# Kernel optimization log

Hardware: AMD Instinct MI355X
Metric: run time of the kernel (lower is better)

## Reference

```python
import jax, jax.numpy as jnp
import numpy as np

EMBED_DIM = 768
NUM_HEADS = 12
HEAD_DIM = EMBED_DIM // NUM_HEADS


def setup_inputs() -> dict:
    key = jax.random.key(0)
    k_x, k_wqkv, k_bqkv, k_wo, k_bo = jax.random.split(key, 5)
    B, S, D = 4, 2048, EMBED_DIM
    bound = 1.0 / np.sqrt(D)
    x = jax.random.normal(k_x, (B, S, D), dtype=jnp.float32)
    # nn.Linear weights: torch stores [out, in]; we keep same layout and use x @ W.T
    W_qkv = jax.random.uniform(k_wqkv, (3 * D, D), jnp.float32, -bound, bound)
    b_qkv = jax.random.uniform(k_bqkv, (3 * D,), jnp.float32, -bound, bound)
    W_out = jax.random.uniform(k_wo, (D, D), jnp.float32, -bound, bound)
    b_out = jax.random.uniform(k_bo, (D,), jnp.float32, -bound, bound)
    return {"x": x, "W_qkv": W_qkv, "b_qkv": b_qkv, "W_out": W_out, "b_out": b_out}


def reference(x, W_qkv, b_qkv, W_out, b_out):
    B, S, D = x.shape
    H, Hd = NUM_HEADS, HEAD_DIM
    qkv = x @ W_qkv.T + b_qkv                       # [B,S,3D]
    qkv = qkv.reshape(B, S, H, 3 * Hd).transpose(0, 2, 1, 3)  # [B,H,S,3Hd]
    q, k, v = jnp.split(qkv, 3, axis=-1)            # each [B,H,S,Hd]
    scale = Hd ** -0.5
    scores = jnp.einsum("bhsd,bhtd->bhst", q, k) * scale  # [B,H,S,S]
    weights = jax.nn.softmax(scores, axis=-1)
    ctx = jnp.einsum("bhst,bhtd->bhsd", weights, v)       # [B,H,S,Hd]
    ctx = ctx.transpose(0, 2, 1, 3).reshape(B, S, D)      # [B,S,D]
    return ctx @ W_out.T + b_out
```

## Files before the change

### kernel.cpp

```cpp
#include <hip/hip_runtime.h>
#include <hip/hip_bf16.h>
#include <stdint.h>
#include <math.h>

typedef unsigned short u16;
typedef __attribute__((ext_vector_type(8))) short short8;
typedef __attribute__((ext_vector_type(4))) float f32x4;
typedef __attribute__((ext_vector_type(2))) unsigned int uint2v;

#define NB 4
#define NS 2048
#define NH 12
#define HD 64
#define ND 768
#define ND3 2304

#define QSCALE 0.18033688f

__device__ __forceinline__ u16 f2bf(float f) {
    unsigned int u = __float_as_uint(f);
    unsigned int r = u + 0x7fffu + ((u >> 16) & 1u);
    return (u16)(r >> 16);
}

typedef const __attribute__((address_space(1))) unsigned int gu32;
typedef __attribute__((address_space(3))) unsigned int lu32;
__device__ __forceinline__ void async16(const void* g, void* l) {
    __builtin_amdgcn_global_load_lds((gu32*)(uintptr_t)g, (lu32*)(uintptr_t)l, 16, 0, 0);
}

__global__ __launch_bounds__(256) void castk(const float* __restrict__ s, u16* __restrict__ d, int n4) {
    int i = blockIdx.x * 256 + threadIdx.x;
    if (i < n4) {
        float4 v = ((const float4*)s)[i];
        ushort4 o;
        o.x = f2bf(v.x); o.y = f2bf(v.y); o.z = f2bf(v.z); o.w = f2bf(v.w);
        ((ushort4*)d)[i] = o;
    }
}

__global__ __launch_bounds__(256) void gemm_qkv(const u16* __restrict__ A,
                                                const u16* __restrict__ Bw,
                                                const float* __restrict__ bias,
                                                u16* __restrict__ Qg,
                                                u16* __restrict__ Kg,
                                                u16* __restrict__ Vtg) {
    __shared__ u16 lds[8192];
    const int tid = threadIdx.x;
    const int w = tid >> 6, l = tid & 63;
    const int lam = l & 15, quad = l >> 4;
    const int wm = w >> 1, wn = w & 1;
    const int bm = blockIdx.x * 128, bn = blockIdx.y * 128;
    const int K = ND;

    f32x4 acc[4][4];
#pragma unroll
    for (int i = 0; i < 4; i++)
#pragma unroll
        for (int j = 0; j < 4; j++) { f32x4 z = {0.f, 0.f, 0.f, 0.f}; acc[i][j] = z; }

    const u16* gp[4];
    u16* sp[4];
#pragma unroll
    for (int i = 0; i < 4; i++) {
        int c = w * 4 + i;
        if (c < 8) { gp[i] = A + (size_t)(bm + c * 16 + lam) * K + quad * 8; sp[i] = lds + c * 512; }
        else { int nf = c - 8; gp[i] = Bw + (size_t)(bn + nf * 16 + lam) * K + quad * 8; sp[i] = lds + 4096 + nf * 512; }
    }

    for (int k0 = 0; k0 < K; k0 += 32) {
        __syncthreads();
#pragma unroll
        for (int i = 0; i < 4; i++) async16(gp[i] + k0, sp[i]);
        __syncthreads();
        short8 a[4], b[4];
#pragma unroll
        for (int i = 0; i < 4; i++) a[i] = *(const short8*)(lds + (wm * 4 + i) * 512 + l * 8);
#pragma unroll
        for (int i = 0; i < 4; i++) b[i] = *(const short8*)(lds + 4096 + (wn * 4 + i) * 512 + l * 8);
#pragma unroll
        for (int mf = 0; mf < 4; mf++)
#pragma unroll
            for (int nf = 0; nf < 4; nf++)
                acc[mf][nf] = __builtin_amdgcn_mfma_f32_16x16x32_bf16(a[mf], b[nf], acc[mf][nf], 0, 0, 0);
    }

#pragma unroll
    for (int nf = 0; nf < 4; nf++) {
        int n = bn + wn * 64 + nf * 16 + lam;
        float bv = bias[n];
        int hh = n / 192, rem = n % 192;
        int rgn = rem / 64, d = rem % 64;
        if (rgn == 2) {
#pragma unroll
            for (int mf = 0; mf < 4; mf++) {
                int m0 = bm + wm * 64 + mf * 16 + quad * 4;
                int bq = m0 >> 11, s0 = m0 & 2047;
                ushort4 o;
                o.x = f2bf(acc[mf][nf][0] + bv);
                o.y = f2bf(acc[mf][nf][1] + bv);
                o.z = f2bf(acc[mf][nf][2] + bv);
                o.w = f2bf(acc[mf][nf][3] + bv);
                *(ushort4*)(Vtg + ((size_t)((bq * NH + hh) * HD + d)) * NS + s0) = o;
            }
        } else {
            u16* dst = (rgn == 0) ? Qg : Kg;
            const float sc = (rgn == 0) ? QSCALE : 1.0f;
#pragma unroll
            for (int mf = 0; mf < 4; mf++)
#pragma unroll
                for (int r = 0; r < 4; r++) {
                    int m = bm + wm * 64 + mf * 16 + quad * 4 + r;
                    int bq = m >> 11, s = m & 2047;
                    dst[((size_t)((bq * NH + hh) * NS + s)) * HD + d] = f2bf((acc[mf][nf][r] + bv) * sc);
                }
        }
    }
}

__global__ __launch_bounds__(256, 3) void attn(const u16* __restrict__ Qg,
                                               const u16* __restrict__ Kg,
                                               const u16* __restrict__ Vtg,
                                               u16* __restrict__ ctx) {
    __shared__ u16 kt_lds[8192];
    __shared__ u16 vt_lds[8192];
    __shared__ u16 p_lds[9216];
    const int tid = threadIdx.x;
    const int w = tid >> 6, l = tid & 63;
    const int lam = l & 15, quad = l >> 4;
    const int qt = blockIdx.x, bh = blockIdx.y;
    const int b = bh / NH, hd = bh % NH;
    const u16* Qh = Qg + (size_t)bh * NS * HD;
    const u16* Kh = Kg + (size_t)bh * NS * HD;
    const u16* Vh = Vtg + (size_t)bh * HD * NS;

    const int qbase = qt * 128 + w * 32;
    short8 qf[2][2];
#pragma unroll
    for (int g = 0; g < 2; g++) {
        const u16* qp = Qh + (size_t)(qbase + g * 16 + lam) * HD + quad * 8;
        qf[g][0] = *(const short8*)(qp);
        qf[g][1] = *(const short8*)(qp + 32);
    }

    f32x4 ot[2][4];
#pragma unroll
    for (int g = 0; g < 2; g++)
#pragma unroll
        for (int i = 0; i < 4; i++) { f32x4 z = {0.f, 0.f, 0.f, 0.f}; ot[g][i] = z; }
    float lacc[2] = {0.f, 0.f};
    u16* pw = p_lds + w * 2304;

    const u16* kg[4];
    const u16* vg[4];
#pragma unroll
    for (int i = 0; i < 4; i++) {
        int cc = w * 4 + i, fgg = cc >> 1, ks = cc & 1;
        kg[i] = Kh + (size_t)(fgg * 16 + lam) * HD + ks * 32 + quad * 8;
        vg[i] = Vh + (size_t)(w * 16 + lam) * NS + i * 32 + quad * 8;
    }

    for (int kt = 0; kt < 16; kt++) {
        __syncthreads();
#pragma unroll
        for (int i = 0; i < 4; i++) { async16(kg[i], kt_lds + (w * 4 + i) * 512); kg[i] += 128 * HD; }
#pragma unroll
        for (int i = 0; i < 4; i++) { async16(vg[i], vt_lds + (w * 4 + i) * 512); vg[i] += 128; }
        __syncthreads();

#pragma unroll
        for (int hf = 0; hf < 2; hf++) {
            f32x4 st[2][4];
#pragma unroll
            for (int fg = 0; fg < 4; fg++) {
                const int cc = (hf * 4 + fg) * 2;
                short8 ka = *(const short8*)(kt_lds + (cc + 0) * 512 + l * 8);
                short8 kb = *(const short8*)(kt_lds + (cc + 1) * 512 + l * 8);
                f32x4 z0 = {0.f, 0.f, 0.f, 0.f};
                f32x4 z1 = {0.f, 0.f, 0.f, 0.f};
                z0 = __builtin_amdgcn_mfma_f32_16x16x32_bf16(ka, qf[0][0], z0, 0, 0, 0);
                z0 = __builtin_amdgcn_mfma_f32_16x16x32_bf16(kb, qf[0][1], z0, 0, 0, 0);
                z1 = __builtin_amdgcn_mfma_f32_16x16x32_bf16(ka, qf[1][0], z1, 0, 0, 0);
                z1 = __builtin_amdgcn_mfma_f32_16x16x32_bf16(kb, qf[1][1], z1, 0, 0, 0);
                st[0][fg] = z0;
                st[1][fg] = z1;
            }

#pragma unroll
            for (int g = 0; g < 2; g++) {
                u16* pr = pw + (g * 16 + lam) * 72;
                float ls = 0.f;
#pragma unroll
                for (int fg = 0; fg < 4; fg++) {
                    unsigned int u0 = __float_as_uint(__builtin_amdgcn_exp2f(st[g][fg][0]));
                    unsigned int u1 = __float_as_uint(__builtin_amdgcn_exp2f(st[g][fg][1]));
                    unsigned int u2 = __float_as_uint(__builtin_amdgcn_exp2f(st[g][fg][2]));
                    unsigned int u3 = __float_as_uint(__builtin_amdgcn_exp2f(st[g][fg][3]));
                    unsigned int t0 = u0 & 0xffff0000u, t1 = u1 & 0xffff0000u;
                    unsigned int t2 = u2 & 0xffff0000u, t3 = u3 & 0xffff0000u;
                    ls += (__uint_as_float(t0) + __uint_as_float(t1)) +
                          (__uint_as_float(t2) + __uint_as_float(t3));
                    uint2v pk;
                    pk.x = (u0 >> 16) | t1;
                    pk.y = (u2 >> 16) | t3;
                    *(uint2v*)(pr + fg * 16 + quad * 4) = pk;
                }
                lacc[g] += ls;
            }

            __builtin_amdgcn_s_waitcnt(0xc07f);

            short8 pf[2][2];
#pragma unroll
            for (int g = 0; g < 2; g++)
#pragma unroll
                for (int ks = 0; ks < 2; ks++)
                    pf[g][ks] = *(const short8*)(pw + (g * 16 + lam) * 72 + ks * 32 + quad * 8);

#pragma unroll
            for (int mf = 0; mf < 4; mf++)
#pragma unroll
                for (int ks = 0; ks < 2; ks++) {
                    short8 va = *(const short8*)(vt_lds + (mf * 4 + hf * 2 + ks) * 512 + l * 8);
                    ot[0][mf] = __builtin_amdgcn_mfma_f32_16x16x32_bf16(va, pf[0][ks], ot[0][mf], 0, 0, 0);
                    ot[1][mf] = __builtin_amdgcn_mfma_f32_16x16x32_bf16(va, pf[1][ks], ot[1][mf], 0, 0, 0);
                }
        }
    }

#pragma unroll
    for (int g = 0; g < 2; g++) {
        float lg = lacc[g];
        lg += __shfl_xor(lg, 16);
        lg += __shfl_xor(lg, 32);
        float inv = 1.0f / lg;
        const int t = qbase + g * 16 + lam;
        size_t obase = (size_t)(b * NS + t) * ND + hd * HD;
#pragma unroll
        for (int mf = 0; mf < 4; mf++) {
            ushort4 o;
            o.x = f2bf(ot[g][mf][0] * inv);
            o.y = f2bf(ot[g][mf][1] * inv);
            o.z = f2bf(ot[g][mf][2] * inv);
            o.w = f2bf(ot[g][mf][3] * inv);
            *(ushort4*)(ctx + obase + mf * 16 + quad * 4) = o;
        }
    }
}

__global__ __launch_bounds__(256) void gemm_out(const u16* __restrict__ A,
                                                const u16* __restrict__ Bw,
                                                const float* __restrict__ bias,
                                                float* __restrict__ out) {
    __shared__ u16 lds[8192];
    const int tid = threadIdx.x;
    const int w = tid >> 6, l = tid & 63;
    const int lam = l & 15, quad = l >> 4;
    const int wm = w >> 1, wn = w & 1;
    const int bm = blockIdx.x * 128, bn = blockIdx.y * 128;
    const int K = ND;

    f32x4 acc[4][4];
#pragma unroll
    for (int i = 0; i < 4; i++)
#pragma unroll
        for (int j = 0; j < 4; j++) { f32x4 z = {0.f, 0.f, 0.f, 0.f}; acc[i][j] = z; }

    const u16* gp[4];
    u16* sp[4];
#pragma unroll
    for (int i = 0; i < 4; i++) {
        int c = w * 4 + i;
        if (c < 8) { gp[i] = A + (size_t)(bm + c * 16 + lam) * K + quad * 8; sp[i] = lds + c * 512; }
        else { int nf = c - 8; gp[i] = Bw + (size_t)(bn + nf * 16 + lam) * K + quad * 8; sp[i] = lds + 4096 + nf * 512; }
    }

    for (int k0 = 0; k0 < K; k0 += 32) {
        __syncthreads();
#pragma unroll
        for (int i = 0; i < 4; i++) async16(gp[i] + k0, sp[i]);
        __syncthreads();
        short8 a[4], b[4];
#pragma unroll
        for (int i = 0; i < 4; i++) a[i] = *(const short8*)(lds + (wm * 4 + i) * 512 + l * 8);
#pragma unroll
        for (int i = 0; i < 4; i++) b[i] = *(const short8*)(lds + 4096 + (wn * 4 + i) * 512 + l * 8);
#pragma unroll
        for (int mf = 0; mf < 4; mf++)
#pragma unroll
            for (int nf = 0; nf < 4; nf++)
                acc[mf][nf] = __builtin_amdgcn_mfma_f32_16x16x32_bf16(a[mf], b[nf], acc[mf][nf], 0, 0, 0);
    }

#pragma unroll
    for (int nf = 0; nf < 4; nf++) {
        int n = bn + wn * 64 + nf * 16 + lam;
        float bv = bias[n];
#pragma unroll
        for (int mf = 0; mf < 4; mf++)
#pragma unroll
            for (int r = 0; r < 4; r++) {
                int m = bm + wm * 64 + mf * 16 + quad * 4 + r;
                out[(size_t)m * ND + n] = acc[mf][nf][r] + bv;
            }
    }
}

extern "C" void kernel_launch(void* const* d_in, const int* in_sizes, int n_in,
                              void* d_out, int out_size, void* d_ws, size_t ws_size,
                              hipStream_t stream) {
    const float* x    = (const float*)d_in[0];
    const float* Wqkv = (const float*)d_in[1];
    const float* bqkv = (const float*)d_in[2];
    const float* Wout = (const float*)d_in[3];
    const float* bout = (const float*)d_in[4];
    float* out = (float*)d_out;

    u16* p = (u16*)d_ws;
    u16* xb    = p; p += 6291456;
    u16* wqkvb = p; p += 1769472;
    u16* wob   = p; p += 589824;
    u16* Qg    = p; p += 6291456;
    u16* Kg    = p; p += 6291456;
    u16* Vtg   = p; p += 6291456;
    u16* ctx   = p; p += 6291456;

    castk<<<6144, 256, 0, stream>>>(x, xb, 1572864);
    castk<<<1728, 256, 0, stream>>>(Wqkv, wqkvb, 442368);
    castk<<<576, 256, 0, stream>>>(Wout, wob, 147456);
    gemm_qkv<<<dim3(64, 18), 256, 0, stream>>>(xb, wqkvb, bqkv, Qg, Kg, Vtg);
    attn<<<dim3(16, 48), 256, 0, stream>>>(Qg, Kg, Vtg, ctx);
    gemm_out<<<dim3(64, 6), 256, 0, stream>>>(ctx, wob, bout, out);
}
```

Measured before the change: 266.1 us.

## Rewrite attention with 32x32 MFMA tiles, register-resident P, and merged cast kernel

The attention kernel now uses 2 waves of 128 threads, each handling 64 query rows. Scores come from 32x32x16 MFMAs, and the exp'd probabilities feed the 32x32x8 PV MFMA straight from registers. This removes the LDS round trip for P and the waitcnt it required. The final row normalisation goes through a small LDS buffer, and the three cast launches are merged into one kernel. In exchange, register pressure per thread rises, each block has fewer waves to hide load latency, and the ctx stores become scalar 2-byte writes.

```diff
diff --git a/kernel.cpp b/kernel.cpp
--- a/kernel.cpp
+++ b/kernel.cpp
@@ -5,8 +5,9 @@
 
 typedef unsigned short u16;
 typedef __attribute__((ext_vector_type(8))) short short8;
+typedef __attribute__((ext_vector_type(4))) short short4v;
 typedef __attribute__((ext_vector_type(4))) float f32x4;
-typedef __attribute__((ext_vector_type(2))) unsigned int uint2v;
+typedef __attribute__((ext_vector_type(16))) float f32x16;
 
 #define NB 4
 #define NS 2048
@@ -29,14 +30,25 @@
     __builtin_amdgcn_global_load_lds((gu32*)(uintptr_t)g, (lu32*)(uintptr_t)l, 16, 0, 0);
 }
 
-__global__ __launch_bounds__(256) void castk(const float* __restrict__ s, u16* __restrict__ d, int n4) {
+#define XN4   1572864
+#define WQN4  442368
+#define WON4  147456
+__global__ __launch_bounds__(256) void castall(const float* __restrict__ x,
+                                               const float* __restrict__ wq,
+                                               const float* __restrict__ wo,
+                                               u16* __restrict__ xb,
+                                               u16* __restrict__ wqb,
+                                               u16* __restrict__ wob) {
     int i = blockIdx.x * 256 + threadIdx.x;
-    if (i < n4) {
-        float4 v = ((const float4*)s)[i];
-        ushort4 o;
-        o.x = f2bf(v.x); o.y = f2bf(v.y); o.z = f2bf(v.z); o.w = f2bf(v.w);
-        ((ushort4*)d)[i] = o;
-    }
+    const float* s; u16* d; int j;
+    if (i < XN4) { s = x; d = xb; j = i; }
+    else if (i < XN4 + WQN4) { s = wq; d = wqb; j = i - XN4; }
+    else if (i < XN4 + WQN4 + WON4) { s = wo; d = wob; j = i - XN4 - WQN4; }
+    else return;
+    float4 v = ((const float4*)s)[j];
+    ushort4 o;
+    o.x = f2bf(v.x); o.y = f2bf(v.y); o.z = f2bf(v.z); o.w = f2bf(v.w);
+    ((ushort4*)d)[j] = o;
 }
 
 __global__ __launch_bounds__(256) void gemm_qkv(const u16* __restrict__ A,
@@ -118,132 +130,116 @@
     }
 }
 
-__global__ __launch_bounds__(256, 3) void attn(const u16* __restrict__ Qg,
+__global__ __launch_bounds__(128, 2) void attn(const u16* __restrict__ Qg,
                                                const u16* __restrict__ Kg,
                                                const u16* __restrict__ Vtg,
                                                u16* __restrict__ ctx) {
     __shared__ u16 kt_lds[8192];
     __shared__ u16 vt_lds[8192];
-    __shared__ u16 p_lds[9216];
+    __shared__ float linv[128];
     const int tid = threadIdx.x;
-    const int w = tid >> 6, l = tid & 63;
-    const int lam = l & 15, quad = l >> 4;
+    const int w = tid >> 6, L = tid & 63;
+    const int r5 = L & 31, h = L >> 5;
     const int qt = blockIdx.x, bh = blockIdx.y;
     const int b = bh / NH, hd = bh % NH;
     const u16* Qh = Qg + (size_t)bh * NS * HD;
     const u16* Kh = Kg + (size_t)bh * NS * HD;
     const u16* Vh = Vtg + (size_t)bh * HD * NS;
 
-    const int qbase = qt * 128 + w * 32;
-    short8 qf[2][2];
-#pragma unroll
-    for (int g = 0; g < 2; g++) {
-        const u16* qp = Qh + (size_t)(qbase + g * 16 + lam) * HD + quad * 8;
-        qf[g][0] = *(const short8*)(qp);
-        qf[g][1] = *(const short8*)(qp + 32);
-    }
-
-    f32x4 ot[2][4];
-#pragma unroll
-    for (int g = 0; g < 2; g++)
-#pragma unroll
-        for (int i = 0; i < 4; i++) { f32x4 z = {0.f, 0.f, 0.f, 0.f}; ot[g][i] = z; }
+    const int qbase = qt * 128 + w * 64;
+
+    short8 qf[2][4];
+#pragma unroll
+    for (int ng = 0; ng < 2; ng++)
+#pragma unroll
+        for (int s = 0; s < 4; s++)
+            qf[ng][s] = *(const short8*)(Qh + (size_t)(qbase + ng * 32 + r5) * HD + s * 16 + h * 8);
+
+    f32x16 ot[2][2];
+#pragma unroll
+    for (int ng = 0; ng < 2; ng++)
+#pragma unroll
+        for (int hg = 0; hg < 2; hg++)
+#pragma unroll
+            for (int r = 0; r < 16; r++) ot[ng][hg][r] = 0.f;
     float lacc[2] = {0.f, 0.f};
-    u16* pw = p_lds + w * 2304;
-
-    const u16* kg[4];
-    const u16* vg[4];
-#pragma unroll
-    for (int i = 0; i < 4; i++) {
-        int cc = w * 4 + i, fgg = cc >> 1, ks = cc & 1;
-        kg[i] = Kh + (size_t)(fgg * 16 + lam) * HD + ks * 32 + quad * 8;
-        vg[i] = Vh + (size_t)(w * 16 + lam) * NS + i * 32 + quad * 8;
+
+    const u16* kgp[8];
+    const u16* vgp[8];
+#pragma unroll
+    for (int i = 0; i < 8; i++) {
+        int c = w * 8 + i, kg = c >> 2, s = c & 3;
+        kgp[i] = Kh + (size_t)(kg * 32 + r5) * HD + s * 16 + h * 8;
+        vgp[i] = Vh + (size_t)(w * 32 + r5) * NS + i * 16 + h * 8;
     }
 
     for (int kt = 0; kt < 16; kt++) {
         __syncthreads();
 #pragma unroll
-        for (int i = 0; i < 4; i++) { async16(kg[i], kt_lds + (w * 4 + i) * 512); kg[i] += 128 * HD; }
-#pragma unroll
-        for (int i = 0; i < 4; i++) { async16(vg[i], vt_lds + (w * 4 + i) * 512); vg[i] += 128; }
-        __syncthreads();
-
-#pragma unroll
-        for (int hf = 0; hf < 2; hf++) {
-            f32x4 st[2][4];
-#pragma unroll
-            for (int fg = 0; fg < 4; fg++) {
-                const int cc = (hf * 4 + fg) * 2;
-                short8 ka = *(const short8*)(kt_lds + (cc + 0) * 512 + l * 8);
-                short8 kb = *(const short8*)(kt_lds + (cc + 1) * 512 + l * 8);
-                f32x4 z0 = {0.f, 0.f, 0.f, 0.f};
-                f32x4 z1 = {0.f, 0.f, 0.f, 0.f};
-                z0 = __builtin_amdgcn_mfma_f32_16x16x32_bf16(ka, qf[0][0], z0, 0, 0, 0);
-                z0 = __builtin_amdgcn_mfma_f32_16x16x32_bf16(kb, qf[0][1], z0, 0, 0, 0);
-                z1 = __builtin_amdgcn_mfma_f32_16x16x32_bf16(ka, qf[1][0], z1, 0, 0, 0);
-                z1 = __builtin_amdgcn_mfma_f32_16x16x32_bf16(kb, qf[1][1], z1, 0, 0, 0);
-                st[0][fg] = z0;
-                st[1][fg] = z1;
-            }
-
-#pragma unroll
-            for (int g = 0; g < 2; g++) {
-                u16* pr = pw + (g * 16 + lam) * 72;
-                float ls = 0.f;
-#pragma unroll
-                for (int fg = 0; fg < 4; fg++) {
-                    unsigned int u0 = __float_as_uint(__builtin_amdgcn_exp2f(st[g][fg][0]));
-                    unsigned int u1 = __float_as_uint(__builtin_amdgcn_exp2f(st[g][fg][1]));
-                    unsigned int u2 = __float_as_uint(__builtin_amdgcn_exp2f(st[g][fg][2]));
-                    unsigned int u3 = __float_as_uint(__builtin_amdgcn_exp2f(st[g][fg][3]));
-                    unsigned int t0 = u0 & 0xffff0000u, t1 = u1 & 0xffff0000u;
-                    unsigned int t2 = u2 & 0xffff0000u, t3 = u3 & 0xffff0000u;
-                    ls += (__uint_as_float(t0) + __uint_as_float(t1)) +
-                          (__uint_as_float(t2) + __uint_as_float(t3));
-                    uint2v pk;
-                    pk.x = (u0 >> 16) | t1;
-                    pk.y = (u2 >> 16) | t3;
-                    *(uint2v*)(pr + fg * 16 + quad * 4) = pk;
+        for (int i = 0; i < 8; i++) { async16(kgp[i], kt_lds + (w * 8 + i) * 512); kgp[i] += 128 * HD; }
+#pragma unroll
+        for (int i = 0; i < 8; i++) { async16(vgp[i], vt_lds + (w * 8 + i) * 512); vgp[i] += 128; }
+        __syncthreads();
+
+#pragma unroll
+        for (int kg = 0; kg < 4; kg++) {
+            f32x16 st[2];
+#pragma unroll
+            for (int r = 0; r < 16; r++) { st[0][r] = 0.f; st[1][r] = 0.f; }
+#pragma unroll
+            for (int s = 0; s < 4; s++) {
+                short8 kf = *(const short8*)(kt_lds + (kg * 4 + s) * 512 + L * 8);
+                st[0] = __builtin_amdgcn_mfma_f32_32x32x16_bf16(kf, qf[0][s], st[0], 0, 0, 0);
+                st[1] = __builtin_amdgcn_mfma_f32_32x32x16_bf16(kf, qf[1][s], st[1], 0, 0, 0);
+            }
+
+#pragma unroll
+            for (int t4 = 0; t4 < 4; t4++) {
+                short4v pf[2];
+#pragma unroll
+                for (int ng = 0; ng < 2; ng++) {
+                    unsigned int u0 = __float_as_uint(__builtin_amdgcn_exp2f(st[ng][4 * t4 + 0]));
+                    unsigned int u1 = __float_as_uint(__builtin_amdgcn_exp2f(st[ng][4 * t4 + 1]));
+                    unsigned int u2 = __float_as_uint(__builtin_amdgcn_exp2f(st[ng][4 * t4 + 2]));
+                    unsigned int u3 = __float_as_uint(__builtin_amdgcn_exp2f(st[ng][4 * t4 + 3]));
+                    lacc[ng] += (__uint_as_float(u0 & 0xffff0000u) + __uint_as_float(u1 & 0xffff0000u)) +
+                                (__uint_as_float(u2 & 0xffff0000u) + __uint_as_float(u3 & 0xffff0000u));
+                    short4v p;
+                    p.x = (short)(u0 >> 16); p.y = (short)(u1 >> 16);
+                    p.z = (short)(u2 >> 16); p.w = (short)(u3 >> 16);
+                    pf[ng] = p;
                 }
-                lacc[g] += ls;
-            }
-
-            __builtin_amdgcn_s_waitcnt(0xc07f);
-
-            short8 pf[2][2];
-#pragma unroll
-            for (int g = 0; g < 2; g++)
-#pragma unroll
-                for (int ks = 0; ks < 2; ks++)
-                    pf[g][ks] = *(const short8*)(pw + (g * 16 + lam) * 72 + ks * 32 + quad * 8);
-
-#pragma unroll
-            for (int mf = 0; mf < 4; mf++)
-#pragma unroll
-                for (int ks = 0; ks < 2; ks++) {
-                    short8 va = *(const short8*)(vt_lds + (mf * 4 + hf * 2 + ks) * 512 + l * 8);
-                    ot[0][mf] = __builtin_amdgcn_mfma_f32_16x16x32_bf16(va, pf[0][ks], ot[0][mf], 0, 0, 0);
-                    ot[1][mf] = __builtin_amdgcn_mfma_f32_16x16x32_bf16(va, pf[1][ks], ot[1][mf], 0, 0, 0);
+                const int t = kg * 4 + t4;
+#pragma unroll
+                for (int hg = 0; hg < 2; hg++) {
+                    short4v vf = *(const short4v*)(vt_lds + hg * 4096 + t * 256 + r5 * 8 + h * 4);
+                    ot[0][hg] = __builtin_amdgcn_mfma_f32_32x32x8bf16_1k(pf[0], vf, ot[0][hg], 0, 0, 0);
+                    ot[1][hg] = __builtin_amdgcn_mfma_f32_32x32x8bf16_1k(pf[1], vf, ot[1][hg], 0, 0, 0);
                 }
+            }
         }
     }
 
-#pragma unroll
-    for (int g = 0; g < 2; g++) {
-        float lg = lacc[g];
-        lg += __shfl_xor(lg, 16);
-        lg += __shfl_xor(lg, 32);
-        float inv = 1.0f / lg;
-        const int t = qbase + g * 16 + lam;
-        size_t obase = (size_t)(b * NS + t) * ND + hd * HD;
-#pragma unroll
-        for (int mf = 0; mf < 4; mf++) {
-            ushort4 o;
-            o.x = f2bf(ot[g][mf][0] * inv);
-            o.y = f2bf(ot[g][mf][1] * inv);
-            o.z = f2bf(ot[g][mf][2] * inv);
-            o.w = f2bf(ot[g][mf][3] * inv);
-            *(ushort4*)(ctx + obase + mf * 16 + quad * 4) = o;
+    float* lp = linv + w * 64;
+#pragma unroll
+    for (int ng = 0; ng < 2; ng++) {
+        float lg = lacc[ng] + __shfl_xor(lacc[ng], 32);
+        lp[ng * 32 + r5] = 1.0f / lg;
+    }
+    __builtin_amdgcn_s_waitcnt(0xc07f);
+
+#pragma unroll
+    for (int ng = 0; ng < 2; ng++) {
+        float sc[16];
+#pragma unroll
+        for (int r = 0; r < 16; r++) sc[r] = lp[ng * 32 + (r & 3) + 8 * (r >> 2) + 4 * h];
+#pragma unroll
+        for (int hg = 0; hg < 2; hg++) {
+#pragma unroll
+            for (int r = 0; r < 16; r++) {
+                int q = qbase + ng * 32 + (r & 3) + 8 * (r >> 2) + 4 * h;
+                ctx[(size_t)(b * NS + q) * ND + hd * HD + hg * 32 + r5] = f2bf(ot[ng][hg][r] * sc[r]);
+            }
         }
     }
 }
@@ -325,10 +321,8 @@
     u16* Vtg   = p; p += 6291456;
     u16* ctx   = p; p += 6291456;
 
-    castk<<<6144, 256, 0, stream>>>(x, xb, 1572864);
-    castk<<<1728, 256, 0, stream>>>(Wqkv, wqkvb, 442368);
-    castk<<<576, 256, 0, stream>>>(Wout, wob, 147456);
+    castall<<<8448, 256, 0, stream>>>(x, Wqkv, Wout, xb, wqkvb, wob);
     gemm_qkv<<<dim3(64, 18), 256, 0, stream>>>(xb, wqkvb, bqkv, Qg, Kg, Vtg);
-    attn<<<dim3(16, 48), 256, 0, stream>>>(Qg, Kg, Vtg, ctx);
+    attn<<<dim3(16, 48), 128, 0, stream>>>(Qg, Kg, Vtg, ctx);
     gemm_out<<<dim3(64, 6), 256, 0, stream>>>(ctx, wob, bout, out);
 }
```

Result: slower. 281.3 us (+5.7%).
